# Kernel tuning notes

Hardware: AMD Instinct MI355X
Metric: run time of the kernel (lower is better)

The kernel has to match this reference:

```python
import jax, jax.numpy as jnp
import numpy as np

B, N, C, T, K = 32, 4096, 768, 1000, 20

def setup_inputs() -> dict:
    key = jax.random.key(0)
    k1, k2, k3, k4 = jax.random.split(key, 4)
    g_feat = jax.random.normal(k1, (B, 1, C), dtype=jnp.float32)
    inp = jax.random.normal(k2, (B, N, C), dtype=jnp.float32)
    tau = jax.random.uniform(k3, (1,), dtype=jnp.float32)
    text_embeddings = jax.random.normal(k4, (T, C), dtype=jnp.float32) * 0.01
    return {"g_feat": g_feat, "input": inp, "tau": tau, "text_embeddings": text_embeddings}


def reference(g_feat, input, tau, text_embeddings):
    feat = input  # [B, N, C]
    # 1x1 conv of global feature against text embeddings -> class logits [B, T]
    vg_logit = jnp.einsum('bc,tc->bt', g_feat[:, 0, :], text_embeddings)
    # top-20 candidate categories per image
    _, indices = jax.lax.top_k(vg_logit, K)              # [B, K]
    agg_text_features = text_embeddings[indices]          # [B, K, C] gather
    # per-pixel logits against the 20 gathered text embeddings
    seg_logit = jnp.exp(tau[0]) * jnp.einsum('bkc,bnc->bkn', agg_text_features, feat)  # [B, K, N]
    # hard (straight-through) softmax over candidate axis (dim=-2)
    y_soft = jax.nn.softmax(seg_logit, axis=-2)
    idx = jnp.argmax(seg_logit, axis=-2)                  # [B, N]
    y_hard = jnp.moveaxis(jax.nn.one_hot(idx, K, dtype=seg_logit.dtype), -1, -2)  # [B, K, N]
    attn = y_hard - jax.lax.stop_gradient(y_soft) + y_soft
    # normalize over pixel axis (assign_eps = 1.0)
    assign_attn = attn / (jnp.sum(attn, axis=-1, keepdims=True) + 1.0)
    # combine: [B, N, K] @ [B, K, C] -> [B, N, C]
    text_grids = jnp.einsum('bkn,bkc->bnc', assign_attn, agg_text_features)
    return text_grids
```

## Files before the change

kernel.cpp:

```cpp
#include <hip/hip_runtime.h>
#include <cfloat>

#define B_ 32
#define N_ 4096
#define C_ 768
#define T_ 1000
#define K_ 20

#define PXB 256
#define PHC 16
#define NPH (C_/PHC)
#define GAP_TH 1e-3f
#define MAXF 16384

typedef float f32x4 __attribute__((ext_vector_type(4)));

__global__ __launch_bounds__(256) void k1_logits(const float* __restrict__ g_feat,
                                                 const float* __restrict__ text,
                                                 double* __restrict__ logits,
                                                 int* __restrict__ cnt,
                                                 int* __restrict__ flagcnt) {
    int b = blockIdx.x;
    int wid = threadIdx.x >> 6, lane = threadIdx.x & 63;
    int t = blockIdx.y * 4 + wid;
    if (b == 0 && blockIdx.y == 0) {
        for (int i = threadIdx.x; i < B_ * K_; i += 256) cnt[i] = 0;
        if (threadIdx.x == 0) flagcnt[0] = 0;
    }
    const float* g = g_feat + b * C_;
    const float* e = text + t * C_;
    double s = 0.0;
    #pragma unroll
    for (int j = 0; j < 12; ++j) {
        int c = lane + 64 * j;
        s += (double)g[c] * (double)e[c];
    }
    #pragma unroll
    for (int m = 32; m; m >>= 1) s += __shfl_xor(s, m);
    if (lane == 0) logits[b * T_ + t] = s;
}

__global__ __launch_bounds__(256) void k1b_topk(const double* __restrict__ logits,
                                                const float* __restrict__ text,
                                                float* __restrict__ agg,
                                                int* __restrict__ sel) {
    __shared__ int ssel[K_];
    int b = blockIdx.x, tid = threadIdx.x, lane = tid & 63;
    if (tid < 64) {
        double v[16];
        #pragma unroll
        for (int j = 0; j < 16; ++j) {
            int t = lane + 64 * j;
            v[j] = (t < T_) ? logits[b * T_ + t] : -DBL_MAX;
        }
        for (int it = 0; it < K_; ++it) {
            double bv = -DBL_MAX; int bi = 0x7fffffff;
            #pragma unroll
            for (int j = 0; j < 16; ++j) {
                int t = lane + 64 * j;
                if (v[j] > bv) { bv = v[j]; bi = t; }
            }
            #pragma unroll
            for (int m = 32; m; m >>= 1) {
                double ov = __shfl_xor(bv, m); int oi = __shfl_xor(bi, m);
                if (ov > bv || (ov == bv && oi < bi)) { bv = ov; bi = oi; }
            }
            if (lane == 0) ssel[it] = bi;
            #pragma unroll
            for (int j = 0; j < 16; ++j) {
                int t = lane + 64 * j;
                if (t == bi) v[j] = -DBL_MAX;
            }
        }
    }
    __syncthreads();
    if (tid < K_) sel[b * K_ + tid] = ssel[tid];
    for (int i = tid; i < K_ * C_; i += 256) {
        int j = i / C_, c = i - j * C_;
        agg[b * K_ * C_ + i] = text[ssel[j] * C_ + c];
    }
}

__global__ __launch_bounds__(128) void k2_argmax(const float* __restrict__ feat,
                                                 const float* __restrict__ agg,
                                                 int* __restrict__ kidx,
                                                 int* __restrict__ cnt,
                                                 int* __restrict__ flagcnt,
                                                 int* __restrict__ flaglist) {
    __shared__ float fbuf[4][PXB * PHC];
    __shared__ float ebuf[4][512];
    __shared__ int scnt[K_];
    int bx = blockIdx.x;
    int b = bx >> 4, tile = bx & 15;
    int n0 = tile * PXB;
    int tid = threadIdx.x, wid = tid >> 6, lane = tid & 63;
    if (tid < K_) scnt[tid] = 0;
    __syncthreads();

    const float* fb = feat + ((size_t)b * N_ + n0) * C_;
    const float* eb = agg + b * (K_ * C_);

    int se = wid * 64 + lane;
    int ce = se < 80 ? se : 79;
    const float* esrc = eb + (ce >> 2) * C_ + (ce & 3) * 4;

    auto stage = [&](int p, int bufi) {
        #pragma unroll
        for (int ii = 0; ii < 8; ++ii) {
            int s = (wid * 8 + ii) * 64 + lane;
            int c = s ^ ((s >> 3) & 7);
            int px = c >> 2, j = c & 3;
            const float* g = fb + (size_t)px * C_ + p * PHC + j * 4;
            float* d = &fbuf[bufi][(wid * 8 + ii) * 256];
            __builtin_amdgcn_global_load_lds((const __attribute__((address_space(1))) void*)g,
                                             (__attribute__((address_space(3))) void*)d, 16, 0, 0);
        }
        {
            const float* g = esrc + p * PHC;
            float* d = &ebuf[bufi][wid * 256];
            __builtin_amdgcn_global_load_lds((const __attribute__((address_space(1))) void*)g,
                                             (__attribute__((address_space(3))) void*)d, 16, 0, 0);
        }
    };

    float acc0[K_], acc1[K_];
    #pragma unroll
    for (int k = 0; k < K_; ++k) { acc0[k] = 0.f; acc1[k] = 0.f; }

    stage(0, 0);
    stage(1, 1);
    stage(2, 2);

    int p0 = tid, p1 = tid + 128;
    #pragma unroll 1
    for (int p = 0; p < NPH; ++p) {
        int bufi = p & 3;
        if (p + 3 < NPH) {
            stage(p + 3, (p + 3) & 3);
            asm volatile("s_waitcnt vmcnt(27)" ::: "memory");
        } else if (p + 2 < NPH) {
            asm volatile("s_waitcnt vmcnt(18)" ::: "memory");
        } else if (p + 1 < NPH) {
            asm volatile("s_waitcnt vmcnt(9)" ::: "memory");
        } else {
            asm volatile("s_waitcnt vmcnt(0)" ::: "memory");
        }
        asm volatile("s_barrier" ::: "memory");

        const float* fB = fbuf[bufi];
        const float* eB = ebuf[bufi];
        f32x4 F0[4], F1[4];
        #pragma unroll
        for (int j = 0; j < 4; ++j) {
            int c0 = p0 * 4 + j, h0 = c0 ^ ((c0 >> 3) & 7);
            F0[j] = *(const f32x4*)(fB + h0 * 4);
            int c1 = p1 * 4 + j, h1 = c1 ^ ((c1 >> 3) & 7);
            F1[j] = *(const f32x4*)(fB + h1 * 4);
        }
        #pragma unroll
        for (int k = 0; k < K_; ++k) {
            float a0 = acc0[k], a1 = acc1[k];
            #pragma unroll
            for (int j = 0; j < 4; ++j) {
                f32x4 e = *(const f32x4*)(eB + (k * 4 + j) * 4);
                a0 = fmaf(F0[j].x, e.x, a0); a0 = fmaf(F0[j].y, e.y, a0);
                a0 = fmaf(F0[j].z, e.z, a0); a0 = fmaf(F0[j].w, e.w, a0);
                a1 = fmaf(F1[j].x, e.x, a1); a1 = fmaf(F1[j].y, e.y, a1);
                a1 = fmaf(F1[j].z, e.z, a1); a1 = fmaf(F1[j].w, e.w, a1);
            }
            acc0[k] = a0; acc1[k] = a1;
        }
        asm volatile("s_barrier" ::: "memory");
    }

    #pragma unroll
    for (int q = 0; q < 2; ++q) {
        float* acc = q ? acc1 : acc0;
        float m1 = acc[0]; int i1 = 0; float m2 = -FLT_MAX;
        #pragma unroll
        for (int k = 1; k < K_; ++k) {
            float v = acc[k];
            if (v > m1) { m2 = m1; m1 = v; i1 = k; }
            else if (v > m2) m2 = v;
        }
        int n = n0 + tid + q * 128;
        kidx[b * N_ + n] = i1;
        atomicAdd(&scnt[i1], 1);
        if (m1 - m2 < GAP_TH) {
            int pos = atomicAdd(flagcnt, 1);
            if (pos < MAXF) flaglist[pos] = b * N_ + n;
        }
    }
    __syncthreads();
    if (tid < K_) atomicAdd(&cnt[b * K_ + tid], scnt[tid]);
}

__global__ __launch_bounds__(256) void k25_refine(const float* __restrict__ feat,
                                                  const float* __restrict__ agg,
                                                  int* __restrict__ kidx,
                                                  int* __restrict__ cnt,
                                                  const int* __restrict__ flagcnt,
                                                  const int* __restrict__ flaglist) {
    int wid = threadIdx.x >> 6, lane = threadIdx.x & 63;
    int wg = blockIdx.x * 4 + wid;
    int nf = flagcnt[0]; if (nf > MAXF) nf = MAXF;
    for (int e = wg; e < nf; e += gridDim.x * 4) {
        int pix = flaglist[e];
        int b = pix >> 12;
        const float* fr = feat + (size_t)pix * C_;
        const float* ebase = agg + b * K_ * C_;
        double fd[12];
        #pragma unroll
        for (int j = 0; j < 12; ++j) fd[j] = (double)fr[lane + 64 * j];
        double best = -DBL_MAX; int bi = 0;
        for (int k = 0; k < K_; ++k) {
            const float* er = ebase + k * C_;
            double s = 0.0;
            #pragma unroll
            for (int j = 0; j < 12; ++j) s += fd[j] * (double)er[lane + 64 * j];
            #pragma unroll
            for (int m = 32; m; m >>= 1) s += __shfl_xor(s, m);
            if (s > best) { best = s; bi = k; }
        }
        if (lane == 0) {
            int old = kidx[pix];
            if (old != bi) {
                kidx[pix] = bi;
                atomicSub(&cnt[b * K_ + old], 1);
                atomicAdd(&cnt[b * K_ + bi], 1);
            }
        }
    }
}

__global__ __launch_bounds__(256) void k4_out(const float* __restrict__ agg,
                                              const int* __restrict__ cnt,
                                              const int* __restrict__ kidx,
                                              float* __restrict__ out) {
    int wid = threadIdx.x >> 6, lane = threadIdx.x & 63;
    int wg = blockIdx.x * 4 + wid;
    int base = wg * 8;
    int b = base >> 12;
    int kk[8];
    #pragma unroll
    for (int i = 0; i < 8; ++i) kk[i] = kidx[base + i];
    float sc[8];
    #pragma unroll
    for (int i = 0; i < 8; ++i) sc[i] = 1.0f / ((float)cnt[b * K_ + kk[i]] + 1.0f);
    const f32x4* agg4 = (const f32x4*)agg;
    f32x4* out4 = (f32x4*)out;
    #pragma unroll
    for (int i = 0; i < 8; ++i) {
        const f32x4* a4 = agg4 + (size_t)(b * K_ + kk[i]) * (C_ / 4);
        f32x4* o4 = out4 + (size_t)(base + i) * (C_ / 4);
        #pragma unroll
        for (int j = 0; j < 3; ++j) {
            f32x4 v = a4[lane + 64 * j];
            v *= sc[i];
            o4[lane + 64 * j] = v;
        }
    }
}

extern "C" void kernel_launch(void* const* d_in, const int* in_sizes, int n_in,
                              void* d_out, int out_size, void* d_ws, size_t ws_size,
                              hipStream_t stream) {
    const float* g_feat = (const float*)d_in[0];
    const float* feat   = (const float*)d_in[1];
    const float* text   = (const float*)d_in[3];
    float* out = (float*)d_out;

    char* ws = (char*)d_ws;
    double* logits = (double*)(ws + 0);
    float*  agg    = (float*) (ws + 262144);
    int*    sel    = (int*)   (ws + 2228224);
    int*    cnt    = (int*)   (ws + 2230784);
    int*    flagc  = (int*)   (ws + 2233344);
    int*    flagl  = (int*)   (ws + 2233408);
    int*    kidx   = (int*)   (ws + 2301504);

    k1_logits<<<dim3(32, 250), 256, 0, stream>>>(g_feat, text, logits, cnt, flagc);
    k1b_topk<<<32, 256, 0, stream>>>(logits, text, agg, sel);
    k2_argmax<<<32 * 16, 128, 0, stream>>>(feat, agg, kidx, cnt, flagc, flagl);
    k25_refine<<<64, 256, 0, stream>>>(feat, agg, kidx, cnt, flagc, flagl);
    k4_out<<<4096, 256, 0, stream>>>(agg, cnt, kidx, out);
}
```

Baseline: 312.7 us.

## Fuse argmax, refine and output kernels with grid-wide barrier

Merges the argmax, the near-tie refinement and the output write into one persistent kernel of 512 blocks. Ties are refined in-block through a wave ballot instead of a global flag list, and a grid-wide atomic barrier waits for the per-class counts before each block writes its own output tile. Each block now uses 256 threads with one pixel per thread, so the per-thread staging loads are halved. This removes two kernel launches and the global kidx and flag-list round trips. In exchange it relies on all 512 blocks being co-resident for the spin barrier and gives each thread fewer accumulators to reuse the loaded embeddings against.

After: 447.4 us. +43.1%, slower.

```diff
diff --git a/kernel.cpp b/kernel.cpp
--- a/kernel.cpp
+++ b/kernel.cpp
@@ -10,8 +10,8 @@
 #define PXB 256
 #define PHC 16
 #define NPH (C_/PHC)
+#define NBLK 512
 #define GAP_TH 1e-3f
-#define MAXF 16384
 
 typedef float f32x4 __attribute__((ext_vector_type(4)));
 
@@ -19,13 +19,13 @@
                                                  const float* __restrict__ text,
                                                  double* __restrict__ logits,
                                                  int* __restrict__ cnt,
-                                                 int* __restrict__ flagcnt) {
+                                                 int* __restrict__ bar) {
     int b = blockIdx.x;
     int wid = threadIdx.x >> 6, lane = threadIdx.x & 63;
     int t = blockIdx.y * 4 + wid;
     if (b == 0 && blockIdx.y == 0) {
         for (int i = threadIdx.x; i < B_ * K_; i += 256) cnt[i] = 0;
-        if (threadIdx.x == 0) flagcnt[0] = 0;
+        if (threadIdx.x == 0) bar[0] = 0;
     }
     const float* g = g_feat + b * C_;
     const float* e = text + t * C_;
@@ -42,8 +42,7 @@
 
 __global__ __launch_bounds__(256) void k1b_topk(const double* __restrict__ logits,
                                                 const float* __restrict__ text,
-                                                float* __restrict__ agg,
-                                                int* __restrict__ sel) {
+                                                float* __restrict__ agg) {
     __shared__ int ssel[K_];
     int b = blockIdx.x, tid = threadIdx.x, lane = tid & 63;
     if (tid < 64) {
@@ -74,74 +73,72 @@
         }
     }
     __syncthreads();
-    if (tid < K_) sel[b * K_ + tid] = ssel[tid];
     for (int i = tid; i < K_ * C_; i += 256) {
         int j = i / C_, c = i - j * C_;
         agg[b * K_ * C_ + i] = text[ssel[j] * C_ + c];
     }
 }
 
-__global__ __launch_bounds__(128) void k2_argmax(const float* __restrict__ feat,
-                                                 const float* __restrict__ agg,
-                                                 int* __restrict__ kidx,
-                                                 int* __restrict__ cnt,
-                                                 int* __restrict__ flagcnt,
-                                                 int* __restrict__ flaglist) {
+__global__ __launch_bounds__(256, 2) void k24_fused(const float* __restrict__ feat,
+                                                    const float* __restrict__ agg,
+                                                    int* __restrict__ cnt,
+                                                    int* __restrict__ bar,
+                                                    float* __restrict__ out) {
     __shared__ float fbuf[4][PXB * PHC];
     __shared__ float ebuf[4][512];
-    __shared__ int scnt[K_];
+    __shared__ int   kidxl[PXB];
+    __shared__ float scs[K_];
+    __shared__ int   scnt[K_];
     int bx = blockIdx.x;
     int b = bx >> 4, tile = bx & 15;
     int n0 = tile * PXB;
     int tid = threadIdx.x, wid = tid >> 6, lane = tid & 63;
     if (tid < K_) scnt[tid] = 0;
-    __syncthreads();
 
     const float* fb = feat + ((size_t)b * N_ + n0) * C_;
     const float* eb = agg + b * (K_ * C_);
 
-    int se = wid * 64 + lane;
-    int ce = se < 80 ? se : 79;
+    int ce = (wid & 1) * 40 + lane; if (ce > 79) ce = 79;
     const float* esrc = eb + (ce >> 2) * C_ + (ce & 3) * 4;
+    int cl = lane ^ ((lane >> 3) & 7);
 
     auto stage = [&](int p, int bufi) {
         #pragma unroll
-        for (int ii = 0; ii < 8; ++ii) {
-            int s = (wid * 8 + ii) * 64 + lane;
-            int c = s ^ ((s >> 3) & 7);
+        for (int ii = 0; ii < 4; ++ii) {
+            int q = wid * 4 + ii;
+            int c = q * 64 + cl;
             int px = c >> 2, j = c & 3;
             const float* g = fb + (size_t)px * C_ + p * PHC + j * 4;
-            float* d = &fbuf[bufi][(wid * 8 + ii) * 256];
+            float* d = &fbuf[bufi][q * 256];
             __builtin_amdgcn_global_load_lds((const __attribute__((address_space(1))) void*)g,
                                              (__attribute__((address_space(3))) void*)d, 16, 0, 0);
         }
         {
             const float* g = esrc + p * PHC;
-            float* d = &ebuf[bufi][wid * 256];
+            float* d = &ebuf[bufi][(wid & 1) * 160];
             __builtin_amdgcn_global_load_lds((const __attribute__((address_space(1))) void*)g,
                                              (__attribute__((address_space(3))) void*)d, 16, 0, 0);
         }
     };
 
-    float acc0[K_], acc1[K_];
-    #pragma unroll
-    for (int k = 0; k < K_; ++k) { acc0[k] = 0.f; acc1[k] = 0.f; }
+    float acc[K_];
+    #pragma unroll
+    for (int k = 0; k < K_; ++k) acc[k] = 0.f;
 
     stage(0, 0);
     stage(1, 1);
     stage(2, 2);
 
-    int p0 = tid, p1 = tid + 128;
     #pragma unroll 1
     for (int p = 0; p < NPH; ++p) {
         int bufi = p & 3;
         if (p + 3 < NPH) {
             stage(p + 3, (p + 3) & 3);
-            asm volatile("s_waitcnt vmcnt(27)" ::: "memory");
+            asm volatile("s_waitcnt vmcnt(15)" ::: "memory");
         } else if (p + 2 < NPH) {
-            asm volatile("s_waitcnt vmcnt(18)" ::: "memory");
+            asm volatile("s_waitcnt vmcnt(10)" ::: "memory");
         } else if (p + 1 < NPH) {
-            asm volatile("s_waitcnt vmcnt(9)" ::: "memory");
+            asm volatile("s_waitcnt vmcnt(5)" ::: "memory");
         } else {
             asm volatile("s_waitcnt vmcnt(0)" ::: "memory");
         }
@@ -149,72 +146,47 @@
 
         const float* fB = fbuf[bufi];
         const float* eB = ebuf[bufi];
-        f32x4 F0[4], F1[4];
+        f32x4 F[4];
         #pragma unroll
         for (int j = 0; j < 4; ++j) {
-            int c0 = p0 * 4 + j, h0 = c0 ^ ((c0 >> 3) & 7);
-            F0[j] = *(const f32x4*)(fB + h0 * 4);
-            int c1 = p1 * 4 + j, h1 = c1 ^ ((c1 >> 3) & 7);
-            F1[j] = *(const f32x4*)(fB + h1 * 4);
+            int c = tid * 4 + j, h = c ^ ((c >> 3) & 7);
+            F[j] = *(const f32x4*)(fB + h * 4);
         }
         #pragma unroll
         for (int k = 0; k < K_; ++k) {
-            float a0 = acc0[k], a1 = acc1[k];
+            float a = acc[k];
             #pragma unroll
             for (int j = 0; j < 4; ++j) {
                 f32x4 e = *(const f32x4*)(eB + (k * 4 + j) * 4);
-                a0 = fmaf(F0[j].x, e.x, a0); a0 = fmaf(F0[j].y, e.y, a0);
-                a0 = fmaf(F0[j].z, e.z, a0); a0 = fmaf(F0[j].w, e.w, a0);
-                a1 = fmaf(F1[j].x, e.x, a1); a1 = fmaf(F1[j].y, e.y, a1);
-                a1 = fmaf(F1[j].z, e.z, a1); a1 = fmaf(F1[j].w, e.w, a1);
-            }
-            acc0[k] = a0; acc1[k] = a1;
+                a = fmaf(F[j].x, e.x, a);
+                a = fmaf(F[j].y, e.y, a);
+                a = fmaf(F[j].z, e.z, a);
+                a = fmaf(F[j].w, e.w, a);
+            }
+            acc[k] = a;
         }
         asm volatile("s_barrier" ::: "memory");
     }
 
-    #pragma unroll
-    for (int q = 0; q < 2; ++q) {
-        float* acc = q ? acc1 : acc0;
-        float m1 = acc[0]; int i1 = 0; float m2 = -FLT_MAX;
-        #pragma unroll
-        for (int k = 1; k < K_; ++k) {
-            float v = acc[k];
-            if (v > m1) { m2 = m1; m1 = v; i1 = k; }
-            else if (v > m2) m2 = v;
-        }
-        int n = n0 + tid + q * 128;
-        kidx[b * N_ + n] = i1;
-        atomicAdd(&scnt[i1], 1);
-        if (m1 - m2 < GAP_TH) {
-            int pos = atomicAdd(flagcnt, 1);
-            if (pos < MAXF) flaglist[pos] = b * N_ + n;
-        }
-    }
-    __syncthreads();
-    if (tid < K_) atomicAdd(&cnt[b * K_ + tid], scnt[tid]);
-}
-
-__global__ __launch_bounds__(256) void k25_refine(const float* __restrict__ feat,
-                                                  const float* __restrict__ agg,
-                                                  int* __restrict__ kidx,
-                                                  int* __restrict__ cnt,
-                                                  const int* __restrict__ flagcnt,
-                                                  const int* __restrict__ flaglist) {
-    int wid = threadIdx.x >> 6, lane = threadIdx.x & 63;
-    int wg = blockIdx.x * 4 + wid;
-    int nf = flagcnt[0]; if (nf > MAXF) nf = MAXF;
-    for (int e = wg; e < nf; e += gridDim.x * 4) {
-        int pix = flaglist[e];
-        int b = pix >> 12;
-        const float* fr = feat + (size_t)pix * C_;
-        const float* ebase = agg + b * K_ * C_;
+    float m1 = acc[0]; int i1 = 0; float m2 = -FLT_MAX;
+    #pragma unroll
+    for (int k = 1; k < K_; ++k) {
+        float v = acc[k];
+        if (v > m1) { m2 = m1; m1 = v; i1 = k; }
+        else if (v > m2) m2 = v;
+    }
+
+    unsigned long long mask = __ballot(m1 - m2 < GAP_TH);
+    while (mask) {
+        int l = __ffsll(mask) - 1; mask &= mask - 1;
+        int px = wid * 64 + l;
+        const float* fr = feat + ((size_t)b * N_ + n0 + px) * C_;
         double fd[12];
         #pragma unroll
         for (int j = 0; j < 12; ++j) fd[j] = (double)fr[lane + 64 * j];
         double best = -DBL_MAX; int bi = 0;
         for (int k = 0; k < K_; ++k) {
-            const float* er = ebase + k * C_;
+            const float* er = eb + k * C_;
             double s = 0.0;
             #pragma unroll
             for (int j = 0; j < 12; ++j) s += fd[j] * (double)er[lane + 64 * j];
@@ -222,42 +194,48 @@
             for (int m = 32; m; m >>= 1) s += __shfl_xor(s, m);
             if (s > best) { best = s; bi = k; }
         }
-        if (lane == 0) {
-            int old = kidx[pix];
-            if (old != bi) {
-                kidx[pix] = bi;
-                atomicSub(&cnt[b * K_ + old], 1);
-                atomicAdd(&cnt[b * K_ + bi], 1);
-            }
-        }
-    }
-}
-
-__global__ __launch_bounds__(256) void k4_out(const float* __restrict__ agg,
-                                              const int* __restrict__ cnt,
-                                              const int* __restrict__ kidx,
-                                              float* __restrict__ out) {
-    int wid = threadIdx.x >> 6, lane = threadIdx.x & 63;
-    int wg = blockIdx.x * 4 + wid;
-    int base = wg * 8;
-    int b = base >> 12;
-    int kk[8];
-    #pragma unroll
-    for (int i = 0; i < 8; ++i) kk[i] = kidx[base + i];
-    float sc[8];
-    #pragma unroll
-    for (int i = 0; i < 8; ++i) sc[i] = 1.0f / ((float)cnt[b * K_ + kk[i]] + 1.0f);
+        if (lane == l) i1 = bi;
+    }
+
+    kidxl[tid] = i1;
+    atomicAdd(&scnt[i1], 1);
+    __syncthreads();
+    if (tid < K_) atomicAdd(&cnt[b * K_ + tid], scnt[tid]);
+    __syncthreads();
+
+    if (tid == 0) {
+        __hip_atomic_fetch_add(bar, 1, __ATOMIC_ACQ_REL, __HIP_MEMORY_SCOPE_AGENT);
+        while (__hip_atomic_load(bar, __ATOMIC_ACQUIRE, __HIP_MEMORY_SCOPE_AGENT) < NBLK)
+            __builtin_amdgcn_s_sleep(1);
+    }
+    __syncthreads();
+
+    if (tid < K_) {
+        int cv = __hip_atomic_load(&cnt[b * K_ + tid], __ATOMIC_RELAXED, __HIP_MEMORY_SCOPE_AGENT);
+        scs[tid] = 1.0f / ((float)cv + 1.0f);
+    }
+    __syncthreads();
+
     const f32x4* agg4 = (const f32x4*)agg;
-    f32x4* out4 = (f32x4*)out;
-    #pragma unroll
-    for (int i = 0; i < 8; ++i) {
-        const f32x4* a4 = agg4 + (size_t)(b * K_ + kk[i]) * (C_ / 4);
-        f32x4* o4 = out4 + (size_t)(base + i) * (C_ / 4);
-        #pragma unroll
-        for (int j = 0; j < 3; ++j) {
-            f32x4 v = a4[lane + 64 * j];
-            v *= sc[i];
-            o4[lane + 64 * j] = v;
+    f32x4* out4 = (f32x4*)out + (size_t)(b * N_ + n0) * (C_ / 4);
+    #pragma unroll 1
+    for (int i = 0; i < 64; i += 4) {
+        int px0 = wid * 64 + i;
+        int kks[4]; float s4[4];
+        #pragma unroll
+        for (int t = 0; t < 4; ++t) { kks[t] = kidxl[px0 + t]; s4[t] = scs[kks[t]]; }
+        f32x4 v[4][3];
+        #pragma unroll
+        for (int t = 0; t < 4; ++t) {
+            const f32x4* a4 = agg4 + (size_t)(b * K_ + kks[t]) * (C_ / 4);
+            #pragma unroll
+            for (int j = 0; j < 3; ++j) v[t][j] = a4[lane + 64 * j];
+        }
+        #pragma unroll
+        for (int t = 0; t < 4; ++t) {
+            #pragma unroll
+            for (int j = 0; j < 3; ++j)
+                out4[(size_t)(px0 + t) * (C_ / 4) + lane + 64 * j] = v[t][j] * s4[t];
         }
     }
 }
@@ -273,15 +251,10 @@
     char* ws = (char*)d_ws;
     double* logits = (double*)(ws + 0);
     float*  agg    = (float*) (ws + 262144);
-    int*    sel    = (int*)   (ws + 2228224);
     int*    cnt    = (int*)   (ws + 2230784);
-    int*    flagc  = (int*)   (ws + 2233344);
-    int*    flagl  = (int*)   (ws + 2233408);
-    int*    kidx   = (int*)   (ws + 2301504);
-
-    k1_logits<<<dim3(32, 250), 256, 0, stream>>>(g_feat, text, logits, cnt, flagc);
-    k1b_topk<<<32, 256, 0, stream>>>(logits, text, agg, sel);
-    k2_argmax<<<32 * 16, 128, 0, stream>>>(feat, agg, kidx, cnt, flagc, flagl);
-    k25_refine<<<64, 256, 0, stream>>>(feat, agg, kidx, cnt, flagc, flagl);
-    k4_out<<<4096, 256, 0, stream>>>(agg, cnt, kidx, out);
-}
+    int*    bar    = (int*)   (ws + 2233344);
+
+    k1_logits<<<dim3(32, 250), 256, 0, stream>>>(g_feat, text, logits, cnt, bar);
+    k1b_topk<<<32, 256, 0, stream>>>(logits, text, agg);
+    k24_fused<<<NBLK, 256, 0, stream>>>(feat, agg, cnt, bar, out);
+}
```

## Restructure argmax kernel to one pixel per thread with smaller channel phases

Applied to the files above, without the earlier changes.

The argmax kernel now uses 256 threads per block, each handling one pixel instead of two. Each pipeline phase covers 8 channels instead of 16, and the staging loads and wait counts are adjusted to match. This cuts accumulator registers and LDS per block, so more blocks can be resident to hide the latency of streaming the feature map. In exchange it runs twice as many phases with their barriers, and each feature load is reused across fewer pixels. The unused top-k index output is also dropped.

Measured after the change: 326.5 us. 1.04x slower.

```diff
diff --git a/kernel.cpp b/kernel.cpp
--- a/kernel.cpp
+++ b/kernel.cpp
@@ -8,7 +8,7 @@
 #define K_ 20
 
 #define PXB 256
-#define PHC 16
+#define PHC 8
 #define NPH (C_/PHC)
 #define GAP_TH 1e-3f
 #define MAXF 16384
@@ -42,8 +42,7 @@
 
 __global__ __launch_bounds__(256) void k1b_topk(const double* __restrict__ logits,
                                                 const float* __restrict__ text,
-                                                float* __restrict__ agg,
-                                                int* __restrict__ sel) {
+                                                float* __restrict__ agg) {
     __shared__ int ssel[K_];
     int b = blockIdx.x, tid = threadIdx.x, lane = tid & 63;
     if (tid < 64) {
@@ -74,21 +73,20 @@
         }
     }
     __syncthreads();
-    if (tid < K_) sel[b * K_ + tid] = ssel[tid];
     for (int i = tid; i < K_ * C_; i += 256) {
         int j = i / C_, c = i - j * C_;
         agg[b * K_ * C_ + i] = text[ssel[j] * C_ + c];
     }
 }
 
-__global__ __launch_bounds__(128) void k2_argmax(const float* __restrict__ feat,
-                                                 const float* __restrict__ agg,
-                                                 int* __restrict__ kidx,
-                                                 int* __restrict__ cnt,
-                                                 int* __restrict__ flagcnt,
-                                                 int* __restrict__ flaglist) {
+__global__ __launch_bounds__(256, 4) void k2_argmax(const float* __restrict__ feat,
+                                                    const float* __restrict__ agg,
+                                                    int* __restrict__ kidx,
+                                                    int* __restrict__ cnt,
+                                                    int* __restrict__ flagcnt,
+                                                    int* __restrict__ flaglist) {
     __shared__ float fbuf[4][PXB * PHC];
-    __shared__ float ebuf[4][512];
+    __shared__ float ebuf[4][256];
     __shared__ int scnt[K_];
     int bx = blockIdx.x;
     int b = bx >> 4, tile = bx & 15;
@@ -100,48 +98,49 @@
     const float* fb = feat + ((size_t)b * N_ + n0) * C_;
     const float* eb = agg + b * (K_ * C_);
 
-    int se = wid * 64 + lane;
-    int ce = se < 80 ? se : 79;
-    const float* esrc = eb + (ce >> 2) * C_ + (ce & 3) * 4;
+    int ce = lane < 40 ? lane : 39;
+    const float* esrc = eb + (ce >> 1) * C_ + (ce & 1) * 4;
 
     auto stage = [&](int p, int bufi) {
         #pragma unroll
-        for (int ii = 0; ii < 8; ++ii) {
-            int s = (wid * 8 + ii) * 64 + lane;
+        for (int ii = 0; ii < 2; ++ii) {
+            int q = (wid * 2 + ii) * 64;
+            int s = q + lane;
             int c = s ^ ((s >> 3) & 7);
-            int px = c >> 2, j = c & 3;
-            const float* g = fb + (size_t)px * C_ + p * PHC + j * 4;
-            float* d = &fbuf[bufi][(wid * 8 + ii) * 256];
+            int px = c >> 1, half = c & 1;
+            const float* g = fb + (size_t)px * C_ + p * PHC + half * 4;
+            float* d = &fbuf[bufi][q * 4];
             __builtin_amdgcn_global_load_lds((const __attribute__((address_space(1))) void*)g,
                                              (__attribute__((address_space(3))) void*)d, 16, 0, 0);
         }
         {
             const float* g = esrc + p * PHC;
-            float* d = &ebuf[bufi][wid * 256];
+            float* d = &ebuf[bufi][0];
             __builtin_amdgcn_global_load_lds((const __attribute__((address_space(1))) void*)g,
                                              (__attribute__((address_space(3))) void*)d, 16, 0, 0);
         }
     };
 
-    float acc0[K_], acc1[K_];
-    #pragma unroll
-    for (int k = 0; k < K_; ++k) { acc0[k] = 0.f; acc1[k] = 0.f; }
+    float acc[K_];
+    #pragma unroll
+    for (int k = 0; k < K_; ++k) acc[k] = 0.f;
 
     stage(0, 0);
     stage(1, 1);
     stage(2, 2);
 
-    int p0 = tid, p1 = tid + 128;
+    int c0 = tid * 2;
+    int h0 = c0 ^ ((c0 >> 3) & 7);
     #pragma unroll 1
     for (int p = 0; p < NPH; ++p) {
         int bufi = p & 3;
         if (p + 3 < NPH) {
             stage(p + 3, (p + 3) & 3);
-            asm volatile("s_waitcnt vmcnt(27)" ::: "memory");
+            asm volatile("s_waitcnt vmcnt(9)" ::: "memory");
         } else if (p + 2 < NPH) {
-            asm volatile("s_waitcnt vmcnt(18)" ::: "memory");
+            asm volatile("s_waitcnt vmcnt(6)" ::: "memory");
         } else if (p + 1 < NPH) {
-            asm volatile("s_waitcnt vmcnt(9)" ::: "memory");
+            asm volatile("s_waitcnt vmcnt(3)" ::: "memory");
         } else {
             asm volatile("s_waitcnt vmcnt(0)" ::: "memory");
         }
@@ -149,47 +148,35 @@
 
         const float* fB = fbuf[bufi];
         const float* eB = ebuf[bufi];
-        f32x4 F0[4], F1[4];
-        #pragma unroll
-        for (int j = 0; j < 4; ++j) {
-            int c0 = p0 * 4 + j, h0 = c0 ^ ((c0 >> 3) & 7);
-            F0[j] = *(const f32x4*)(fB + h0 * 4);
-            int c1 = p1 * 4 + j, h1 = c1 ^ ((c1 >> 3) & 7);
-            F1[j] = *(const f32x4*)(fB + h1 * 4);
-        }
+        f32x4 F0 = *(const f32x4*)(fB + h0 * 4);
+        f32x4 F1 = *(const f32x4*)(fB + (h0 ^ 1) * 4);
         #pragma unroll
         for (int k = 0; k < K_; ++k) {
-            float a0 = acc0[k], a1 = acc1[k];
-            #pragma unroll
-            for (int j = 0; j < 4; ++j) {
-                f32x4 e = *(const f32x4*)(eB + (k * 4 + j) * 4);
-                a0 = fmaf(F0[j].x, e.x, a0); a0 = fmaf(F0[j].y, e.y, a0);
-                a0 = fmaf(F0[j].z, e.z, a0); a0 = fmaf(F0[j].w, e.w, a0);
-                a1 = fmaf(F1[j].x, e.x, a1); a1 = fmaf(F1[j].y, e.y, a1);
-                a1 = fmaf(F1[j].z, e.z, a1); a1 = fmaf(F1[j].w, e.w, a1);
-            }
-            acc0[k] = a0; acc1[k] = a1;
+            f32x4 e0 = *(const f32x4*)(eB + (k * 2 + 0) * 4);
+            f32x4 e1 = *(const f32x4*)(eB + (k * 2 + 1) * 4);
+            float a = acc[k];
+            a = fmaf(F0.x, e0.x, a); a = fmaf(F0.y, e0.y, a);
+            a = fmaf(F0.z, e0.z, a); a = fmaf(F0.w, e0.w, a);
+            a = fmaf(F1.x, e1.x, a); a = fmaf(F1.y, e1.y, a);
+            a = fmaf(F1.z, e1.z, a); a = fmaf(F1.w, e1.w, a);
+            acc[k] = a;
         }
         asm volatile("s_barrier" ::: "memory");
     }
 
-    #pragma unroll
-    for (int q = 0; q < 2; ++q) {
-        float* acc = q ? acc1 : acc0;
-        float m1 = acc[0]; int i1 = 0; float m2 = -FLT_MAX;
-        #pragma unroll
-        for (int k = 1; k < K_; ++k) {
-            float v = acc[k];
-            if (v > m1) { m2 = m1; m1 = v; i1 = k; }
-            else if (v > m2) m2 = v;
-        }
-        int n = n0 + tid + q * 128;
-        kidx[b * N_ + n] = i1;
-        atomicAdd(&scnt[i1], 1);
-        if (m1 - m2 < GAP_TH) {
-            int pos = atomicAdd(flagcnt, 1);
-            if (pos < MAXF) flaglist[pos] = b * N_ + n;
-        }
+    float m1 = acc[0]; int i1 = 0; float m2 = -FLT_MAX;
+    #pragma unroll
+    for (int k = 1; k < K_; ++k) {
+        float v = acc[k];
+        if (v > m1) { m2 = m1; m1 = v; i1 = k; }
+        else if (v > m2) m2 = v;
+    }
+    int n = n0 + tid;
+    kidx[b * N_ + n] = i1;
+    atomicAdd(&scnt[i1], 1);
+    if (m1 - m2 < GAP_TH) {
+        int pos = atomicAdd(flagcnt, 1);
+        if (pos < MAXF) flaglist[pos] = b * N_ + n;
     }
     __syncthreads();
     if (tid < K_) atomicAdd(&cnt[b * K_ + tid], scnt[tid]);
@@ -273,15 +260,14 @@
     char* ws = (char*)d_ws;
     double* logits = (double*)(ws + 0);
     float*  agg    = (float*) (ws + 262144);
-    int*    sel    = (int*)   (ws + 2228224);
     int*    cnt    = (int*)   (ws + 2230784);
     int*    flagc  = (int*)   (ws + 2233344);
     int*    flagl  = (int*)   (ws + 2233408);
     int*    kidx   = (int*)   (ws + 2301504);
 
     k1_logits<<<dim3(32, 250), 256, 0, stream>>>(g_feat, text, logits, cnt, flagc);
-    k1b_topk<<<32, 256, 0, stream>>>(logits, text, agg, sel);
-    k2_argmax<<<32 * 16, 128, 0, stream>>>(feat, agg, kidx, cnt, flagc, flagl);
+    k1b_topk<<<32, 256, 0, stream>>>(logits, text, agg);
+    k2_argmax<<<32 * 16, 256, 0, stream>>>(feat, agg, kidx, cnt, flagc, flagl);
     k25_refine<<<64, 256, 0, stream>>>(feat, agg, kidx, cnt, flagc, flagl);
     k4_out<<<4096, 256, 0, stream>>>(agg, cnt, kidx, out);
 }
```
